# Kernel tuning notes

Measured on AMD Instinct MI355X. Metric: run time of the kernel, lower is better.

The kernel has to match this reference:

```python
import jax, jax.numpy as jnp
import numpy as np

L = 6       # label_num (number of semantic 'experts')
P = 3       # number of triplane planes
CPL = 32    # channels per label per plane
HID = 64    # decoder hidden width
BOX_WARP = 2.0

_PLANES = np.array([[[1, 0, 0], [0, 1, 0], [0, 0, 1]],
                    [[1, 0, 0], [0, 0, 1], [0, 1, 0]],
                    [[0, 0, 1], [0, 1, 0], [1, 0, 0]]], dtype=np.float32)
_INV_PLANES = np.linalg.inv(_PLANES)


def grid_sample_one(img, grid):
    """Bilinear grid_sample, align_corners=False, zeros padding.
    img: [C,H,W], grid: [M,2] (x,y) in [-1,1] -> [C,M]."""
    C, H, W = img.shape
    x = (grid[:, 0] + 1.0) * (W * 0.5) - 0.5
    y = (grid[:, 1] + 1.0) * (H * 0.5) - 0.5
    x0f = jnp.floor(x)
    y0f = jnp.floor(y)
    wx1 = x - x0f
    wy1 = y - y0f
    wx0 = 1.0 - wx1
    wy0 = 1.0 - wy1
    x0 = x0f.astype(jnp.int32)
    y0 = y0f.astype(jnp.int32)

    def gather(xi, yi):
        valid = ((xi >= 0) & (xi < W) & (yi >= 0) & (yi < H)).astype(img.dtype)
        v = img[:, jnp.clip(yi, 0, H - 1), jnp.clip(xi, 0, W - 1)]
        return v * valid[None, :]

    return (gather(x0, y0) * (wx0 * wy0)[None]
            + gather(x0 + 1, y0) * (wx1 * wy0)[None]
            + gather(x0, y0 + 1) * (wx0 * wy1)[None]
            + gather(x0 + 1, y0 + 1) * (wx1 * wy1)[None])


def _forward(planes, coordinates, w1, b1, w2, b2, beta):
    N, _, C, H, W = planes.shape
    pf = planes.reshape(N, P, L, C // L, H, W)  # per-label triplane features
    inv = jnp.asarray(_INV_PLANES)

    def delta_fn(coords):
        scaled = coords * (2.0 / BOX_WARP)
        # project onto the three planes: [N,P,M,2]
        proj = jnp.einsum('nmi,pij->npmj', scaled, inv)[..., :2]
        # gather features: [N,P,L,c,M]
        feats = jax.vmap(jax.vmap(
            lambda imgs, g: jax.vmap(lambda im: grid_sample_one(im, g))(imgs)
        ))(pf, proj)
        feat = feats.mean(1).transpose(0, 1, 3, 2)  # mean over planes -> [N,L,M,c]
        h = jax.nn.softplus(jnp.einsum('nlmc,lch->nlmh', feat, w1) + b1[:, None, :])
        o = jnp.einsum('nlmh,lho->nlmo', h, w2) + b2[:, None, :]  # [N,L,M,5]
        sigma_l = o[..., 0:1]  # per-label delta-SDF
        rgb_l = o[..., 1:4]    # per-label rgb logits
        delta = sigma_l.sum(1)  # [N,M,1]
        return delta, (sigma_l, rgb_l)

    # delta SDF and its gradient wrt coordinates (sdf_gradient in torch)
    delta, vjp_fn, aux = jax.vjp(delta_fn, coordinates, has_aux=True)
    sigma_l, rgb_l = aux
    grad_cano = vjp_fn(jnp.ones_like(delta))[0]  # [N,M,3]

    # stand-in for deformer.deformer.query_sdf: sphere SDF (detached in all uses)
    r = jnp.linalg.norm(coordinates, axis=-1)
    smpl_sdf = r - 0.5                              # [N,M]
    smpl_grad = coordinates / (r[..., None] + 1e-8)  # analytic sdf gradient

    sdf = jax.lax.stop_gradient(smpl_sdf)[..., None] + delta  # [N,M,1]
    s = sigma_l + jax.lax.stop_gradient(smpl_sdf)[:, None, :, None]  # [N,L,M,1]
    local_sigma = jax.nn.sigmoid(-s / beta) / beta  # sdf_activation
    sigma = local_sigma.sum(1)                      # [N,M,1]
    semantic = local_sigma / (sigma[:, None] + 1e-8)  # [N,L,M,1]
    rgb = jax.nn.sigmoid((rgb_l * semantic).sum(1)) * (1.0 + 2 * 0.001) - 0.001  # [N,M,3]
    rgb_out = jnp.concatenate([rgb, semantic[..., 0].transpose(0, 2, 1)], -1)  # [N,M,3+L]
    grad = grad_cano + jax.lax.stop_gradient(smpl_grad)
    # pack: sdf(1) | sigma(1) | rgb+semantics(3+L) | grad(3) | grad_cano(3) -> [N,M,17]
    return jnp.concatenate([sdf, sigma, rgb_out, grad, grad_cano], -1)


def setup_inputs() -> dict:
    key = jax.random.key(0)
    ks = jax.random.split(key, 4)
    N, M, HP = 2, 65536, 256
    planes = jax.random.normal(ks[0], (N, P, L * CPL, HP, HP), jnp.float32) * 0.1
    coordinates = jax.random.uniform(ks[1], (N, M, 3), jnp.float32, -1.0, 1.0)
    w1 = jax.random.normal(ks[2], (L, CPL, HID), jnp.float32) * (1.0 / np.sqrt(CPL))
    b1 = jnp.zeros((L, HID), jnp.float32)
    w2 = jax.random.normal(ks[3], (L, HID, 5), jnp.float32) * (1.0 / np.sqrt(HID))
    b2 = jnp.zeros((L, 5), jnp.float32)
    beta = jnp.full((1,), 0.1, jnp.float32)  # sigmoid_beta parameter
    return {"planes": planes, "coordinates": coordinates, "w1": w1, "b1": b1,
            "w2": w2, "b2": b2, "beta": beta}


def reference(planes, coordinates, w1, b1, w2, b2, beta):
    return _forward(planes, coordinates, w1, b1, w2, b2, beta)
```

## Files before the change

kernel.cpp:

```cpp
#include <hip/hip_runtime.h>
#include <math.h>

#define P_   3
#define L_   6
#define CPL_ 32
#define C_   192
#define HID_ 64

__device__ __forceinline__ float bf2f(unsigned short u) {
    return __uint_as_float(((unsigned int)u) << 16);
}
__device__ __forceinline__ float fexp(float x)  { return __expf(x); }
__device__ __forceinline__ float frcp(float x)  { return __builtin_amdgcn_rcpf(x); }
__device__ __forceinline__ float flog1p(float e){ return __logf(1.0f + e); }

__global__ __launch_bounds__(256) void transpose_kernel(
    const float* __restrict__ in, unsigned short* __restrict__ out)
{
    __shared__ __align__(16) float tile[32][196];
    const int np   = blockIdx.x >> 11;
    const int pix0 = (blockIdx.x & 2047) << 5;
    const float* src = in + (size_t)np * C_ * 65536;
    uint4* dst4 = (uint4*)(out + (size_t)np * 65536 * C_);
    const int t = threadIdx.x;

    #pragma unroll
    for (int it = 0; it < 6; ++it) {
        int idx = it * 256 + t;
        int Cc  = idx >> 3;
        int pq  = idx & 7;
        float4 fv = *(const float4*)&src[(size_t)Cc * 65536 + pix0 + 4 * pq];
        tile[4 * pq + 0][Cc] = fv.x;
        tile[4 * pq + 1][Cc] = fv.y;
        tile[4 * pq + 2][Cc] = fv.z;
        tile[4 * pq + 3][Cc] = fv.w;
    }
    __syncthreads();
    #pragma unroll
    for (int it = 0; it < 3; ++it) {
        int idx = it * 256 + t;
        int c8  = idx % 24;
        int px  = idx / 24;
        float4 a = *(const float4*)&tile[px][8 * c8];
        float4 b = *(const float4*)&tile[px][8 * c8 + 4];
        unsigned int u0 = __float_as_uint(a.x), u1 = __float_as_uint(a.y);
        unsigned int u2 = __float_as_uint(a.z), u3 = __float_as_uint(a.w);
        unsigned int u4 = __float_as_uint(b.x), u5 = __float_as_uint(b.y);
        unsigned int u6 = __float_as_uint(b.z), u7 = __float_as_uint(b.w);
        u0 = (u0 + 0x7fffu + ((u0 >> 16) & 1)) >> 16;
        u1 = (u1 + 0x7fffu + ((u1 >> 16) & 1)) >> 16;
        u2 = (u2 + 0x7fffu + ((u2 >> 16) & 1)) >> 16;
        u3 = (u3 + 0x7fffu + ((u3 >> 16) & 1)) >> 16;
        u4 = (u4 + 0x7fffu + ((u4 >> 16) & 1)) >> 16;
        u5 = (u5 + 0x7fffu + ((u5 >> 16) & 1)) >> 16;
        u6 = (u6 + 0x7fffu + ((u6 >> 16) & 1)) >> 16;
        u7 = (u7 + 0x7fffu + ((u7 >> 16) & 1)) >> 16;
        uint4 pk;
        pk.x = u0 | (u1 << 16);
        pk.y = u2 | (u3 << 16);
        pk.z = u4 | (u5 << 16);
        pk.w = u6 | (u7 << 16);
        dst4[(size_t)(pix0 + px) * 24 + c8] = pk;
    }
}

__global__ __launch_bounds__(512)
__attribute__((amdgpu_waves_per_eu(2, 4))) void point2(
    const unsigned short* __restrict__ planes_bf,
    const float* __restrict__ coords,
    const float* __restrict__ w1,
    const float* __restrict__ b1,
    const float* __restrict__ w2,
    const float* __restrict__ b2,
    const float* __restrict__ betap,
    float* __restrict__ out)
{
    extern __shared__ float sm[];
    float* w1s = sm;
    float* b1s = sm + 12288;
    float* w2s = sm + 12672;
    float* b2s = sm + 14592;
    float* cds = sm + 14624;
    float* pwv = sm + 14816;

    const int tid  = threadIdx.x;
    const int wave = tid >> 6;
    const int lane = tid & 63;
    float* feat_s = pwv + wave * 600;
    float* dz_s   = feat_s + 192;
    float* o_s    = dz_s + 384;

    #pragma unroll
    for (int it = 0; it < 24; ++it) {
        int idx = it * 512 + tid;
        int cg = idx >> 6, h = idx & 63;
        w1s[cg * 64 + (h ^ ((cg & 31) << 1))] = w1[idx];
    }
    if (tid < 384) b1s[tid] = b1[tid];
    #pragma unroll
    for (int it = 0; it < 4; ++it) {
        int idx = it * 512 + tid;
        if (idx < 1920) w2s[idx] = w2[idx];
    }
    if (tid < 30)  b2s[tid] = b2[tid];
    if (tid < 192) cds[tid] = coords[(size_t)blockIdx.x * 192 + tid];
    __syncthreads();

    float b1r[L_], b2r[L_];
    #pragma unroll
    for (int l = 0; l < L_; ++l) {
        b1r[l] = b1s[l * HID_ + lane];
        b2r[l] = b2s[l * 5 + (lane & 3)];
    }

    const float rbeta = frcp(betap[0]);
    const int gw = blockIdx.x * 8 + wave;
    const int n  = blockIdx.x >> 10;
    const unsigned short* pb = planes_bf + (size_t)n * 3 * 65536 * C_;
    const int Cx = (lane & 31) << 1;

    #pragma unroll 1
    for (int i = 0; i < 8; ++i) {
        const int pt3 = (wave * 8 + i) * 3;
        const float cx = cds[pt3 + 0];
        const float cy = cds[pt3 + 1];
        const float cz = cds[pt3 + 2];
        const float pjx[3] = {cx, cx, cz};
        const float pjy[3] = {cy, cz, cy};

        float wx0[3], wx1[3], wy0[3], wy1[3], vm[3][4];
        int   pixi[3][4];
        #pragma unroll
        for (int p = 0; p < 3; ++p) {
            float px = (pjx[p] + 1.0f) * 128.0f - 0.5f;
            float py = (pjy[p] + 1.0f) * 128.0f - 0.5f;
            float x0f = floorf(px), y0f = floorf(py);
            wx1[p] = px - x0f; wx0[p] = 1.0f - wx1[p];
            wy1[p] = py - y0f; wy0[p] = 1.0f - wy1[p];
            int x0 = (int)x0f, y0 = (int)y0f;
            int x1 = x0 + 1,  y1 = y0 + 1;
            int xc0 = min(max(x0, 0), 255), xc1 = min(max(x1, 0), 255);
            int yc0 = min(max(y0, 0), 255), yc1 = min(max(y1, 0), 255);
            float vx0 = (x0 >= 0 && x0 < 256) ? 1.f : 0.f;
            float vx1 = (x1 >= 0 && x1 < 256) ? 1.f : 0.f;
            float vy0 = (y0 >= 0 && y0 < 256) ? 1.f : 0.f;
            float vy1 = (y1 >= 0 && y1 < 256) ? 1.f : 0.f;
            pixi[p][0] = yc0 * 256 + xc0; vm[p][0] = vx0 * vy0;
            pixi[p][1] = yc0 * 256 + xc1; vm[p][1] = vx1 * vy0;
            pixi[p][2] = yc1 * 256 + xc0; vm[p][2] = vx0 * vy1;
            pixi[p][3] = yc1 * 256 + xc1; vm[p][3] = vx1 * vy1;
        }

        unsigned short us[3][4][3];
        #pragma unroll
        for (int p = 0; p < 3; ++p) {
            const unsigned short* bp = pb + (size_t)p * 65536 * C_;
            #pragma unroll
            for (int j = 0; j < 4; ++j) {
                const unsigned short* a = bp + (size_t)pixi[p][j] * C_ + lane;
                us[p][j][0] = a[0];
                us[p][j][1] = a[64];
                us[p][j][2] = a[128];
            }
        }

        float gxS[3], gyS[3], gzS[3];
        #pragma unroll
        for (int k = 0; k < 3; ++k) {
            float f = 0.f;
            float gxc[3], gyc[3];
            #pragma unroll
            for (int p = 0; p < 3; ++p) {
                float g0 = bf2f(us[p][0][k]) * vm[p][0];
                float g1 = bf2f(us[p][1][k]) * vm[p][1];
                float g2 = bf2f(us[p][2][k]) * vm[p][2];
                float g3 = bf2f(us[p][3][k]) * vm[p][3];
                f += wx0[p] * wy0[p] * g0 + wx1[p] * wy0[p] * g1
                   + wx0[p] * wy1[p] * g2 + wx1[p] * wy1[p] * g3;
                gxc[p] = wy0[p] * (g1 - g0) + wy1[p] * (g3 - g2);
                gyc[p] = wx0[p] * (g2 - g0) + wx1[p] * (g3 - g1);
            }
            gxS[k] = gxc[0] + gxc[1];
            gyS[k] = gyc[0] + gyc[2];
            gzS[k] = gyc[1] + gxc[2];
            feat_s[lane + 64 * k] = f * (1.0f / 3.0f);
        }
        asm volatile("s_waitcnt lgkmcnt(0)" ::: "memory");

        #pragma unroll
        for (int l = 0; l < L_; ++l) {
            const float* w2l = &w2s[(l * HID_ + lane) * 5];
            float w20 = w2l[0], w21 = w2l[1], w22 = w2l[2], w23 = w2l[3];

            float z0 = b1r[l], z1 = 0.f;
            #pragma unroll
            for (int q = 0; q < 8; ++q) {
                float4 fv = *(const float4*)&feat_s[l * CPL_ + 4 * q];
                z0 = fmaf(fv.x, w1s[((l*CPL_ + 4*q + 0) << 6) + (lane ^ (((4*q + 0) & 31) << 1))], z0);
                z1 = fmaf(fv.y, w1s[((l*CPL_ + 4*q + 1) << 6) + (lane ^ (((4*q + 1) & 31) << 1))], z1);
                z0 = fmaf(fv.z, w1s[((l*CPL_ + 4*q + 2) << 6) + (lane ^ (((4*q + 2) & 31) << 1))], z0);
                z1 = fmaf(fv.w, w1s[((l*CPL_ + 4*q + 3) << 6) + (lane ^ (((4*q + 3) & 31) << 1))], z1);
            }
            float z  = z0 + z1;
            float e  = fexp(-fabsf(z));
            float sp = fmaxf(z, 0.f) + flog1p(e);
            float d  = frcp(1.0f + e);
            float sg = ((z > 0.f) ? 1.0f : e) * d;
            dz_s[l * HID_ + lane] = sg * w20;

            float o0 = sp * w20, o1 = sp * w21, o2 = sp * w22, o3 = sp * w23;
            float u  = (lane & 1) ? o1 : o0;
            float uw = (lane & 1) ? o0 : o1;
            u += __shfl_xor(uw, 1, 64);
            float v  = (lane & 1) ? o3 : o2;
            float vw = (lane & 1) ? o2 : o3;
            v += __shfl_xor(vw, 1, 64);
            float tt = (lane & 2) ? v : u;
            float tw = (lane & 2) ? u : v;
            tt += __shfl_xor(tw, 2, 64);
            tt += __shfl_xor(tt, 4, 64);
            tt += __shfl_xor(tt, 8, 64);
            tt += __shfl_xor(tt, 16, 64);
            tt += __shfl_xor(tt, 32, 64);
            if ((lane >> 2) == l)
                o_s[lane] = tt + b2r[l];
        }
        asm volatile("s_waitcnt lgkmcnt(0)" ::: "memory");

        float df[3];
        #pragma unroll
        for (int k = 0; k < 3; ++k) {
            const int cg = lane + 64 * k;
            const float* wr  = &w1s[cg << 6];
            const float* dzr = &dz_s[(cg >> 5) * HID_];
            float a0 = 0.f, a1 = 0.f;
            #pragma unroll
            for (int h2 = 0; h2 < 32; ++h2) {
                float2 wv = *(const float2*)&wr[(2 * h2) ^ Cx];
                float2 dv = *(const float2*)&dzr[2 * h2];
                a0 = fmaf(wv.x, dv.x, a0);
                a1 = fmaf(wv.y, dv.y, a1);
            }
            df[k] = a0 + a1;
        }

        float gx = 0.f, gy = 0.f, gz = 0.f;
        #pragma unroll
        for (int k = 0; k < 3; ++k) {
            gx = fmaf(df[k], gxS[k], gx);
            gy = fmaf(df[k], gyS[k], gy);
            gz = fmaf(df[k], gzS[k], gz);
        }
        #pragma unroll
        for (int s = 1; s < 64; s <<= 1) {
            gx += __shfl_xor(gx, s, 64);
            gy += __shfl_xor(gy, s, 64);
            gz += __shfl_xor(gz, s, 64);
        }
        const float F = 128.0f / 3.0f;
        float gcx = F * gx;
        float gcy = F * gy;
        float gcz = F * gz;

        float olev[L_][4];
        #pragma unroll
        for (int l = 0; l < L_; ++l) {
            float4 ov = *(const float4*)&o_s[4 * l];
            olev[l][0] = ov.x; olev[l][1] = ov.y;
            olev[l][2] = ov.z; olev[l][3] = ov.w;
        }

        float r    = sqrtf(cx * cx + cy * cy + cz * cz);
        float smpl = r - 0.5f;
        float delta = 0.f;
        #pragma unroll
        for (int l = 0; l < L_; ++l) delta += olev[l][0];
        float sdf = smpl + delta;

        float ls[L_], sigma = 0.f;
        #pragma unroll
        for (int l = 0; l < L_; ++l) {
            float s = olev[l][0] + smpl;
            ls[l] = frcp(1.0f + fexp(s * rbeta)) * rbeta;
            sigma += ls[l];
        }
        float inv = frcp(sigma + 1e-8f);
        float sem[L_];
        #pragma unroll
        for (int l = 0; l < L_; ++l) sem[l] = ls[l] * inv;

        float r0 = 0.f, r1 = 0.f, r2 = 0.f;
        #pragma unroll
        for (int l = 0; l < L_; ++l) {
            r0 = fmaf(olev[l][1], sem[l], r0);
            r1 = fmaf(olev[l][2], sem[l], r1);
            r2 = fmaf(olev[l][3], sem[l], r2);
        }
        float rgb0 = frcp(1.0f + fexp(-r0)) * 1.002f - 0.001f;
        float rgb1 = frcp(1.0f + fexp(-r1)) * 1.002f - 0.001f;
        float rgb2 = frcp(1.0f + fexp(-r2)) * 1.002f - 0.001f;

        float rinv = frcp(r + 1e-8f);
        if (lane < 17) {
            float v =
                (lane == 0)  ? sdf :
                (lane == 1)  ? sigma :
                (lane == 2)  ? rgb0 :
                (lane == 3)  ? rgb1 :
                (lane == 4)  ? rgb2 :
                (lane == 5)  ? sem[0] :
                (lane == 6)  ? sem[1] :
                (lane == 7)  ? sem[2] :
                (lane == 8)  ? sem[3] :
                (lane == 9)  ? sem[4] :
                (lane == 10) ? sem[5] :
                (lane == 11) ? gcx + cx * rinv :
                (lane == 12) ? gcy + cy * rinv :
                (lane == 13) ? gcz + cz * rinv :
                (lane == 14) ? gcx :
                (lane == 15) ? gcy : gcz;
            out[(size_t)(gw * 8 + i) * 17 + lane] = v;
        }
    }
}

__global__ __launch_bounds__(256, 4) void point_fallback(
    const float* __restrict__ planes_f32,
    const float* __restrict__ coords,
    const float* __restrict__ w1,
    const float* __restrict__ b1,
    const float* __restrict__ w2,
    const float* __restrict__ b2,
    const float* __restrict__ betap,
    float* __restrict__ out)
{
    __shared__ __align__(16) float feat_s[4][C_];
    __shared__ __align__(16) float dz_s[4][L_ * HID_];
    __shared__ __align__(16) float o_s[4][24];

    const int wave  = threadIdx.x >> 6;
    const int lane  = threadIdx.x & 63;
    const int point = blockIdx.x * 4 + wave;
    const int n     = point >> 16;

    const float cx = coords[point * 3 + 0];
    const float cy = coords[point * 3 + 1];
    const float cz = coords[point * 3 + 2];

    const float pjx[3] = {cx, cx, cz};
    const float pjy[3] = {cy, cz, cy};

    float wx0[3], wx1[3], wy0[3], wy1[3];
    int   pixi[3][4];
    float vmk[3][4];
    #pragma unroll
    for (int p = 0; p < 3; ++p) {
        float px = (pjx[p] + 1.0f) * 128.0f - 0.5f;
        float py = (pjy[p] + 1.0f) * 128.0f - 0.5f;
        float x0f = floorf(px), y0f = floorf(py);
        wx1[p] = px - x0f; wx0[p] = 1.0f - wx1[p];
        wy1[p] = py - y0f; wy0[p] = 1.0f - wy1[p];
        int x0 = (int)x0f, y0 = (int)y0f;
        int x1 = x0 + 1,  y1 = y0 + 1;
        int xc0 = min(max(x0, 0), 255), xc1 = min(max(x1, 0), 255);
        int yc0 = min(max(y0, 0), 255), yc1 = min(max(y1, 0), 255);
        float vx0 = (x0 >= 0 && x0 < 256) ? 1.f : 0.f;
        float vx1 = (x1 >= 0 && x1 < 256) ? 1.f : 0.f;
        float vy0 = (y0 >= 0 && y0 < 256) ? 1.f : 0.f;
        float vy1 = (y1 >= 0 && y1 < 256) ? 1.f : 0.f;
        pixi[p][0] = yc0 * 256 + xc0; vmk[p][0] = vx0 * vy0;
        pixi[p][1] = yc0 * 256 + xc1; vmk[p][1] = vx1 * vy0;
        pixi[p][2] = yc1 * 256 + xc0; vmk[p][2] = vx0 * vy1;
        pixi[p][3] = yc1 * 256 + xc1; vmk[p][3] = vx1 * vy1;
    }

    float g[3][4][3];
    #pragma unroll
    for (int p = 0; p < 3; ++p)
        #pragma unroll
        for (int ij = 0; ij < 4; ++ij)
            #pragma unroll
            for (int k = 0; k < 3; ++k) {
                int Cc = lane + 64 * k;
                size_t a = ((size_t)((n * 3 + p) * C_ + Cc)) * 65536 + pixi[p][ij];
                g[p][ij][k] = planes_f32[a] * vmk[p][ij];
            }

    #pragma unroll
    for (int k = 0; k < 3; ++k) {
        float f = 0.f;
        #pragma unroll
        for (int p = 0; p < 3; ++p) {
            f += wx0[p] * wy0[p] * g[p][0][k] + wx1[p] * wy0[p] * g[p][1][k]
               + wx0[p] * wy1[p] * g[p][2][k] + wx1[p] * wy1[p] * g[p][3][k];
        }
        feat_s[wave][lane + 64 * k] = f * (1.0f / 3.0f);
    }
    asm volatile("s_waitcnt lgkmcnt(0)" ::: "memory");

    #pragma unroll
    for (int l = 0; l < L_; ++l) {
        float b1l = b1[l * HID_ + lane];
        const float* w2l = w2 + (l * HID_ + lane) * 5;
        float w20 = w2l[0], w21 = w2l[1], w22 = w2l[2], w23 = w2l[3];

        float z0 = b1l, z1 = 0.f;
        #pragma unroll
        for (int q = 0; q < 8; ++q) {
            float4 fv = *(const float4*)&feat_s[wave][l * CPL_ + 4 * q];
            z0 = fmaf(fv.x, w1[(l * CPL_ + 4 * q + 0) * HID_ + lane], z0);
            z1 = fmaf(fv.y, w1[(l * CPL_ + 4 * q + 1) * HID_ + lane], z1);
            z0 = fmaf(fv.z, w1[(l * CPL_ + 4 * q + 2) * HID_ + lane], z0);
            z1 = fmaf(fv.w, w1[(l * CPL_ + 4 * q + 3) * HID_ + lane], z1);
        }
        float z  = z0 + z1;
        float e  = expf(-fabsf(z));
        float sp = fmaxf(z, 0.f) + log1pf(e);
        float sg = ((z > 0.f) ? 1.0f : e) / (1.0f + e);
        dz_s[wave][l * HID_ + lane] = sg * w20;

        float o0 = sp * w20, o1 = sp * w21, o2 = sp * w22, o3 = sp * w23;
        float u  = (lane & 1) ? o1 : o0;
        float uw = (lane & 1) ? o0 : o1;
        u += __shfl_xor(uw, 1, 64);
        float v  = (lane & 1) ? o3 : o2;
        float vw = (lane & 1) ? o2 : o3;
        v += __shfl_xor(vw, 1, 64);
        float tt = (lane & 2) ? v : u;
        float tw = (lane & 2) ? u : v;
        tt += __shfl_xor(tw, 2, 64);
        tt += __shfl_xor(tt, 4, 64);
        tt += __shfl_xor(tt, 8, 64);
        tt += __shfl_xor(tt, 16, 64);
        tt += __shfl_xor(tt, 32, 64);
        if ((lane >> 2) == l)
            o_s[wave][lane] = tt + b2[l * 5 + (lane & 3)];
    }
    asm volatile("s_waitcnt lgkmcnt(0)" ::: "memory");

    float df[3];
    #pragma unroll
    for (int k = 0; k < 3; ++k) {
        int cg = lane + 64 * k;
        const float* w1r = w1 + cg * HID_;
        const float* dzr = &dz_s[wave][(cg >> 5) * HID_];
        float a0 = 0.f, a1 = 0.f;
        #pragma unroll
        for (int h4 = 0; h4 < 16; ++h4) {
            float4 wv = *(const float4*)(w1r + 4 * h4);
            float4 dv = *(const float4*)(dzr + 4 * h4);
            a0 = fmaf(wv.x, dv.x, a0);
            a1 = fmaf(wv.y, dv.y, a1);
            a0 = fmaf(wv.z, dv.z, a0);
            a1 = fmaf(wv.w, dv.w, a1);
        }
        df[k] = a0 + a1;
    }

    float ax[3] = {0.f, 0.f, 0.f};
    float ay[3] = {0.f, 0.f, 0.f};
    #pragma unroll
    for (int k = 0; k < 3; ++k)
        #pragma unroll
        for (int p = 0; p < 3; ++p) {
            ax[p] = fmaf(df[k], wy0[p] * (g[p][1][k] - g[p][0][k])
                               + wy1[p] * (g[p][3][k] - g[p][2][k]), ax[p]);
            ay[p] = fmaf(df[k], wx0[p] * (g[p][2][k] - g[p][0][k])
                               + wx1[p] * (g[p][3][k] - g[p][1][k]), ay[p]);
        }
    #pragma unroll
    for (int s = 1; s < 64; s <<= 1) {
        ax[0] += __shfl_xor(ax[0], s, 64);
        ax[1] += __shfl_xor(ax[1], s, 64);
        ax[2] += __shfl_xor(ax[2], s, 64);
        ay[0] += __shfl_xor(ay[0], s, 64);
        ay[1] += __shfl_xor(ay[1], s, 64);
        ay[2] += __shfl_xor(ay[2], s, 64);
    }
    const float F = 128.0f / 3.0f;
    float gcx = F * (ax[0] + ax[1]);
    float gcy = F * (ay[0] + ay[2]);
    float gcz = F * (ay[1] + ax[2]);

    const float beta = betap[0];
    float olev[L_][4];
    #pragma unroll
    for (int l = 0; l < L_; ++l) {
        float4 ov = *(const float4*)&o_s[wave][4 * l];
        olev[l][0] = ov.x; olev[l][1] = ov.y;
        olev[l][2] = ov.z; olev[l][3] = ov.w;
    }

    float r    = sqrtf(cx * cx + cy * cy + cz * cz);
    float smpl = r - 0.5f;
    float delta = 0.f;
    #pragma unroll
    for (int l = 0; l < L_; ++l) delta += olev[l][0];
    float sdf = smpl + delta;

    float ls[L_], sigma = 0.f;
    #pragma unroll
    for (int l = 0; l < L_; ++l) {
        float s = olev[l][0] + smpl;
        ls[l] = (1.0f / (1.0f + expf(s / beta))) / beta;
        sigma += ls[l];
    }
    float inv = 1.0f / (sigma + 1e-8f);
    float sem[L_];
    #pragma unroll
    for (int l = 0; l < L_; ++l) sem[l] = ls[l] * inv;

    float r0 = 0.f, r1 = 0.f, r2 = 0.f;
    #pragma unroll
    for (int l = 0; l < L_; ++l) {
        r0 = fmaf(olev[l][1], sem[l], r0);
        r1 = fmaf(olev[l][2], sem[l], r1);
        r2 = fmaf(olev[l][3], sem[l], r2);
    }
    float rgb0 = (1.0f / (1.0f + expf(-r0))) * 1.002f - 0.001f;
    float rgb1 = (1.0f / (1.0f + expf(-r1))) * 1.002f - 0.001f;
    float rgb2 = (1.0f / (1.0f + expf(-r2))) * 1.002f - 0.001f;

    float rinv = 1.0f / (r + 1e-8f);
    if (lane < 17) {
        float v =
            (lane == 0)  ? sdf :
            (lane == 1)  ? sigma :
            (lane == 2)  ? rgb0 :
            (lane == 3)  ? rgb1 :
            (lane == 4)  ? rgb2 :
            (lane == 5)  ? sem[0] :
            (lane == 6)  ? sem[1] :
            (lane == 7)  ? sem[2] :
            (lane == 8)  ? sem[3] :
            (lane == 9)  ? sem[4] :
            (lane == 10) ? sem[5] :
            (lane == 11) ? gcx + cx * rinv :
            (lane == 12) ? gcy + cy * rinv :
            (lane == 13) ? gcz + cz * rinv :
            (lane == 14) ? gcx :
            (lane == 15) ? gcy : gcz;
        out[(size_t)point * 17 + lane] = v;
    }
}

extern "C" void kernel_launch(void* const* d_in, const int* in_sizes, int n_in,
                              void* d_out, int out_size, void* d_ws, size_t ws_size,
                              hipStream_t stream)
{
    const float* planes = (const float*)d_in[0];
    const float* coords = (const float*)d_in[1];
    const float* w1     = (const float*)d_in[2];
    const float* b1     = (const float*)d_in[3];
    const float* w2     = (const float*)d_in[4];
    const float* b2     = (const float*)d_in[5];
    const float* beta   = (const float*)d_in[6];
    float* out = (float*)d_out;

    const size_t need = (size_t)6 * 65536 * C_ * sizeof(unsigned short);
    const int shmem = 19616 * 4;

    if (ws_size >= need) {
        static bool attr_done = false;
        if (!attr_done) {
            (void)hipFuncSetAttribute(reinterpret_cast<const void*>(&point2),
                                      hipFuncAttributeMaxDynamicSharedMemorySize,
                                      shmem);
            attr_done = true;
        }
        unsigned short* tp = (unsigned short*)d_ws;
        transpose_kernel<<<6 * 2048, 256, 0, stream>>>(planes, tp);
        point2<<<2048, 512, shmem, stream>>>(
            tp, coords, w1, b1, w2, b2, beta, out);
    } else {
        point_fallback<<<131072 / 4, 256, 0, stream>>>(
            planes, coords, w1, b1, w2, b2, beta, out);
    }
}
```

Before: 1.009 ms.

## Reorder gradient chain rule, keep w2 in registers, convert to bf16 before transpose

The backward pass no longer computes dz then a separate w1^T·dz per channel. Instead it projects the spatial gradients onto w1 inside the forward hidden-layer loop and accumulates dz times those projections, which removes the second sweep over w1 in LDS and the dz scratch. w2 moves from LDS into registers, and the output reductions for all labels are batched into one shuffle tree. The transpose kernel now converts to bf16 before writing LDS, halving tile size. Occupancy hints go to 4 waves/EU, and the extra FMAs and registers may cause spills.

Result: faster. 836.2 us (-17.1%).

```diff
diff --git a/kernel.cpp b/kernel.cpp
--- a/kernel.cpp
+++ b/kernel.cpp
@@ -10,6 +10,11 @@
 __device__ __forceinline__ float bf2f(unsigned short u) {
     return __uint_as_float(((unsigned int)u) << 16);
 }
+__device__ __forceinline__ unsigned short f2bf(float x) {
+    unsigned int u = __float_as_uint(x);
+    u = (u + 0x7fffu + ((u >> 16) & 1)) >> 16;
+    return (unsigned short)u;
+}
 __device__ __forceinline__ float fexp(float x)  { return __expf(x); }
 __device__ __forceinline__ float frcp(float x)  { return __builtin_amdgcn_rcpf(x); }
 __device__ __forceinline__ float flog1p(float e){ return __logf(1.0f + e); }
@@ -17,12 +22,13 @@
 __global__ __launch_bounds__(256) void transpose_kernel(
     const float* __restrict__ in, unsigned short* __restrict__ out)
 {
-    __shared__ __align__(16) float tile[32][196];
+    __shared__ unsigned int tile32[32 * 97 + 4];
     const int np   = blockIdx.x >> 11;
     const int pix0 = (blockIdx.x & 2047) << 5;
     const float* src = in + (size_t)np * C_ * 65536;
     uint4* dst4 = (uint4*)(out + (size_t)np * 65536 * C_);
     const int t = threadIdx.x;
+    unsigned short* tp = (unsigned short*)tile32;
 
     #pragma unroll
     for (int it = 0; it < 6; ++it) {
@@ -30,42 +36,26 @@
         int Cc  = idx >> 3;
         int pq  = idx & 7;
         float4 fv = *(const float4*)&src[(size_t)Cc * 65536 + pix0 + 4 * pq];
-        tile[4 * pq + 0][Cc] = fv.x;
-        tile[4 * pq + 1][Cc] = fv.y;
-        tile[4 * pq + 2][Cc] = fv.z;
-        tile[4 * pq + 3][Cc] = fv.w;
+        tp[(4 * pq + 0) * 194 + Cc] = f2bf(fv.x);
+        tp[(4 * pq + 1) * 194 + Cc] = f2bf(fv.y);
+        tp[(4 * pq + 2) * 194 + Cc] = f2bf(fv.z);
+        tp[(4 * pq + 3) * 194 + Cc] = f2bf(fv.w);
     }
     __syncthreads();
     #pragma unroll
     for (int it = 0; it < 3; ++it) {
         int idx = it * 256 + t;
-        int c8  = idx % 24;
+        int c4  = idx % 24;
         int px  = idx / 24;
-        float4 a = *(const float4*)&tile[px][8 * c8];
-        float4 b = *(const float4*)&tile[px][8 * c8 + 4];
-        unsigned int u0 = __float_as_uint(a.x), u1 = __float_as_uint(a.y);
-        unsigned int u2 = __float_as_uint(a.z), u3 = __float_as_uint(a.w);
-        unsigned int u4 = __float_as_uint(b.x), u5 = __float_as_uint(b.y);
-        unsigned int u6 = __float_as_uint(b.z), u7 = __float_as_uint(b.w);
-        u0 = (u0 + 0x7fffu + ((u0 >> 16) & 1)) >> 16;
-        u1 = (u1 + 0x7fffu + ((u1 >> 16) & 1)) >> 16;
-        u2 = (u2 + 0x7fffu + ((u2 >> 16) & 1)) >> 16;
-        u3 = (u3 + 0x7fffu + ((u3 >> 16) & 1)) >> 16;
-        u4 = (u4 + 0x7fffu + ((u4 >> 16) & 1)) >> 16;
-        u5 = (u5 + 0x7fffu + ((u5 >> 16) & 1)) >> 16;
-        u6 = (u6 + 0x7fffu + ((u6 >> 16) & 1)) >> 16;
-        u7 = (u7 + 0x7fffu + ((u7 >> 16) & 1)) >> 16;
+        const unsigned int* rp = tile32 + px * 97 + 4 * c4;
         uint4 pk;
-        pk.x = u0 | (u1 << 16);
-        pk.y = u2 | (u3 << 16);
-        pk.z = u4 | (u5 << 16);
-        pk.w = u6 | (u7 << 16);
-        dst4[(size_t)(pix0 + px) * 24 + c8] = pk;
+        pk.x = rp[0]; pk.y = rp[1]; pk.z = rp[2]; pk.w = rp[3];
+        dst4[(size_t)(pix0 + px) * 24 + c4] = pk;
     }
 }
 
 __global__ __launch_bounds__(512)
-__attribute__((amdgpu_waves_per_eu(2, 4))) void point2(
+__attribute__((amdgpu_waves_per_eu(4, 4))) void point2(
     const unsigned short* __restrict__ planes_bf,
     const float* __restrict__ coords,
     const float* __restrict__ w1,
@@ -78,46 +68,43 @@
     extern __shared__ float sm[];
     float* w1s = sm;
     float* b1s = sm + 12288;
-    float* w2s = sm + 12672;
-    float* b2s = sm + 14592;
-    float* cds = sm + 14624;
-    float* pwv = sm + 14816;
+    float* b2s = sm + 12672;
+    float* cds = sm + 12704;
+    float* pwv = sm + 12896;
 
     const int tid  = threadIdx.x;
     const int wave = tid >> 6;
     const int lane = tid & 63;
-    float* feat_s = pwv + wave * 600;
-    float* dz_s   = feat_s + 192;
-    float* o_s    = dz_s + 384;
-
-    #pragma unroll
-    for (int it = 0; it < 24; ++it) {
+    float* feat_s = pwv + wave * 792;
+    float* gxs    = feat_s + 192;
+    float* gys    = gxs + 192;
+    float* gzs    = gys + 192;
+    float* o_s    = gzs + 192;
+
+    #pragma unroll
+    for (int it = 0; it < 6; ++it) {
         int idx = it * 512 + tid;
-        int cg = idx >> 6, h = idx & 63;
-        w1s[cg * 64 + (h ^ ((cg & 31) << 1))] = w1[idx];
+        ((float4*)w1s)[idx] = ((const float4*)w1)[idx];
     }
     if (tid < 384) b1s[tid] = b1[tid];
-    #pragma unroll
-    for (int it = 0; it < 4; ++it) {
-        int idx = it * 512 + tid;
-        if (idx < 1920) w2s[idx] = w2[idx];
-    }
     if (tid < 30)  b2s[tid] = b2[tid];
     if (tid < 192) cds[tid] = coords[(size_t)blockIdx.x * 192 + tid];
     __syncthreads();
 
     float b1r[L_], b2r[L_];
+    float w2r0[L_], w2r1[L_], w2r2[L_], w2r3[L_];
     #pragma unroll
     for (int l = 0; l < L_; ++l) {
         b1r[l] = b1s[l * HID_ + lane];
         b2r[l] = b2s[l * 5 + (lane & 3)];
+        const float* w2l = w2 + (size_t)(l * HID_ + lane) * 5;
+        w2r0[l] = w2l[0]; w2r1[l] = w2l[1]; w2r2[l] = w2l[2]; w2r3[l] = w2l[3];
     }
 
     const float rbeta = frcp(betap[0]);
     const int gw = blockIdx.x * 8 + wave;
     const int n  = blockIdx.x >> 10;
     const unsigned short* pb = planes_bf + (size_t)n * 3 * 65536 * C_;
-    const int Cx = (lane & 31) << 1;
 
     #pragma unroll 1
     for (int i = 0; i < 8; ++i) {
@@ -164,7 +151,6 @@
             }
         }
 
-        float gxS[3], gyS[3], gzS[3];
         #pragma unroll
         for (int k = 0; k < 3; ++k) {
             float f = 0.f;
@@ -180,35 +166,53 @@
                 gxc[p] = wy0[p] * (g1 - g0) + wy1[p] * (g3 - g2);
                 gyc[p] = wx0[p] * (g2 - g0) + wx1[p] * (g3 - g1);
             }
-            gxS[k] = gxc[0] + gxc[1];
-            gyS[k] = gyc[0] + gyc[2];
-            gzS[k] = gyc[1] + gxc[2];
             feat_s[lane + 64 * k] = f * (1.0f / 3.0f);
+            gxs[lane + 64 * k] = gxc[0] + gxc[1];
+            gys[lane + 64 * k] = gyc[0] + gyc[2];
+            gzs[lane + 64 * k] = gyc[1] + gxc[2];
         }
         asm volatile("s_waitcnt lgkmcnt(0)" ::: "memory");
 
+        float gx = 0.f, gy = 0.f, gz = 0.f;
+        float tl[L_];
         #pragma unroll
         for (int l = 0; l < L_; ++l) {
-            const float* w2l = &w2s[(l * HID_ + lane) * 5];
-            float w20 = w2l[0], w21 = w2l[1], w22 = w2l[2], w23 = w2l[3];
-
             float z0 = b1r[l], z1 = 0.f;
+            float axl = 0.f, ayl = 0.f, azl = 0.f;
             #pragma unroll
             for (int q = 0; q < 8; ++q) {
-                float4 fv = *(const float4*)&feat_s[l * CPL_ + 4 * q];
-                z0 = fmaf(fv.x, w1s[((l*CPL_ + 4*q + 0) << 6) + (lane ^ (((4*q + 0) & 31) << 1))], z0);
-                z1 = fmaf(fv.y, w1s[((l*CPL_ + 4*q + 1) << 6) + (lane ^ (((4*q + 1) & 31) << 1))], z1);
-                z0 = fmaf(fv.z, w1s[((l*CPL_ + 4*q + 2) << 6) + (lane ^ (((4*q + 2) & 31) << 1))], z0);
-                z1 = fmaf(fv.w, w1s[((l*CPL_ + 4*q + 3) << 6) + (lane ^ (((4*q + 3) & 31) << 1))], z1);
+                const int c0 = l * CPL_ + 4 * q;
+                float4 fv  = *(const float4*)&feat_s[c0];
+                float4 gxv = *(const float4*)&gxs[c0];
+                float4 gyv = *(const float4*)&gys[c0];
+                float4 gzv = *(const float4*)&gzs[c0];
+                float wA = w1s[((c0 + 0) << 6) + lane];
+                float wB = w1s[((c0 + 1) << 6) + lane];
+                float wC = w1s[((c0 + 2) << 6) + lane];
+                float wD = w1s[((c0 + 3) << 6) + lane];
+                z0 = fmaf(fv.x, wA, z0);
+                z1 = fmaf(fv.y, wB, z1);
+                z0 = fmaf(fv.z, wC, z0);
+                z1 = fmaf(fv.w, wD, z1);
+                axl = fmaf(wA, gxv.x, axl); axl = fmaf(wB, gxv.y, axl);
+                axl = fmaf(wC, gxv.z, axl); axl = fmaf(wD, gxv.w, axl);
+                ayl = fmaf(wA, gyv.x, ayl); ayl = fmaf(wB, gyv.y, ayl);
+                ayl = fmaf(wC, gyv.z, ayl); ayl = fmaf(wD, gyv.w, ayl);
+                azl = fmaf(wA, gzv.x, azl); azl = fmaf(wB, gzv.y, azl);
+                azl = fmaf(wC, gzv.z, azl); azl = fmaf(wD, gzv.w, azl);
             }
             float z  = z0 + z1;
             float e  = fexp(-fabsf(z));
             float sp = fmaxf(z, 0.f) + flog1p(e);
             float d  = frcp(1.0f + e);
             float sg = ((z > 0.f) ? 1.0f : e) * d;
-            dz_s[l * HID_ + lane] = sg * w20;
-
-            float o0 = sp * w20, o1 = sp * w21, o2 = sp * w22, o3 = sp * w23;
+            float dzl = sg * w2r0[l];
+            gx = fmaf(dzl, axl, gx);
+            gy = fmaf(dzl, ayl, gy);
+            gz = fmaf(dzl, azl, gz);
+
+            float o0 = sp * w2r0[l], o1 = sp * w2r1[l];
+            float o2 = sp * w2r2[l], o3 = sp * w2r3[l];
             float u  = (lane & 1) ? o1 : o0;
             float uw = (lane & 1) ? o0 : o1;
             u += __shfl_xor(uw, 1, 64);
@@ -218,49 +222,37 @@
             float tt = (lane & 2) ? v : u;
             float tw = (lane & 2) ? u : v;
             tt += __shfl_xor(tw, 2, 64);
-            tt += __shfl_xor(tt, 4, 64);
-            tt += __shfl_xor(tt, 8, 64);
-            tt += __shfl_xor(tt, 16, 64);
-            tt += __shfl_xor(tt, 32, 64);
-            if ((lane >> 2) == l)
-                o_s[lane] = tt + b2r[l];
-        }
-        asm volatile("s_waitcnt lgkmcnt(0)" ::: "memory");
-
-        float df[3];
-        #pragma unroll
-        for (int k = 0; k < 3; ++k) {
-            const int cg = lane + 64 * k;
-            const float* wr  = &w1s[cg << 6];
-            const float* dzr = &dz_s[(cg >> 5) * HID_];
-            float a0 = 0.f, a1 = 0.f;
-            #pragma unroll
-            for (int h2 = 0; h2 < 32; ++h2) {
-                float2 wv = *(const float2*)&wr[(2 * h2) ^ Cx];
-                float2 dv = *(const float2*)&dzr[2 * h2];
-                a0 = fmaf(wv.x, dv.x, a0);
-                a1 = fmaf(wv.y, dv.y, a1);
-            }
-            df[k] = a0 + a1;
-        }
-
-        float gx = 0.f, gy = 0.f, gz = 0.f;
-        #pragma unroll
-        for (int k = 0; k < 3; ++k) {
-            gx = fmaf(df[k], gxS[k], gx);
-            gy = fmaf(df[k], gyS[k], gy);
-            gz = fmaf(df[k], gzS[k], gz);
-        }
-        #pragma unroll
-        for (int s = 1; s < 64; s <<= 1) {
+            tl[l] = tt;
+        }
+
+        gx += __shfl_xor(gx, 1, 64);
+        gy += __shfl_xor(gy, 1, 64);
+        gz += __shfl_xor(gz, 1, 64);
+        gx += __shfl_xor(gx, 2, 64);
+        gy += __shfl_xor(gy, 2, 64);
+        gz += __shfl_xor(gz, 2, 64);
+        #pragma unroll
+        for (int s = 4; s < 64; s <<= 1) {
             gx += __shfl_xor(gx, s, 64);
             gy += __shfl_xor(gy, s, 64);
             gz += __shfl_xor(gz, s, 64);
+            tl[0] += __shfl_xor(tl[0], s, 64);
+            tl[1] += __shfl_xor(tl[1], s, 64);
+            tl[2] += __shfl_xor(tl[2], s, 64);
+            tl[3] += __shfl_xor(tl[3], s, 64);
+            tl[4] += __shfl_xor(tl[4], s, 64);
+            tl[5] += __shfl_xor(tl[5], s, 64);
         }
         const float F = 128.0f / 3.0f;
         float gcx = F * gx;
         float gcy = F * gy;
         float gcz = F * gz;
+
+        #pragma unroll
+        for (int l = 0; l < L_; ++l)
+            if ((lane >> 2) == l)
+                o_s[lane] = tl[l] + b2r[l];
+        asm volatile("s_waitcnt lgkmcnt(0)" ::: "memory");
 
         float olev[L_][4];
         #pragma unroll
@@ -558,7 +550,7 @@
     float* out = (float*)d_out;
 
     const size_t need = (size_t)6 * 65536 * C_ * sizeof(unsigned short);
-    const int shmem = 19616 * 4;
+    const int shmem = 19232 * 4;
 
     if (ws_size >= need) {
         static bool attr_done = false;
```
